# Performance work log

Hardware: AMD Instinct MI355X
Metric: run time of the kernel (lower is better)

The kernel has to match this reference:

```python
import jax, jax.numpy as jnp
import numpy as np

N = 50000
E = 800000
IN_DIM = 128
HID = 64
OUT_DIM = 1
NEG_SLOPE = 0.2
EPS = 1e-16


def _glorot(key, shape):
    fan = shape[-1] + (shape[0] if len(shape) > 1 else shape[-1])
    lim = jnp.sqrt(6.0 / fan)
    return jax.random.uniform(key, shape, jnp.float32, -lim, lim)


def setup_inputs() -> dict:
    key = jax.random.key(0)
    ks = jax.random.split(key, 12)
    x = jax.random.normal(ks[0], (N, IN_DIM), jnp.float32)
    edge_index = jax.random.randint(ks[1], (2, E), 0, N, jnp.int64)
    # GATConv layer 1: in=128, out=64, heads=4, concat=True
    W1 = _glorot(ks[2], (4 * HID, IN_DIM))
    att_src1 = _glorot(ks[3], (4, HID))
    att_dst1 = _glorot(ks[4], (4, HID))
    b1 = jnp.zeros((4 * HID,), jnp.float32)
    # GATConv layer 2: in=256, out=64, heads=1, concat=True
    W2 = _glorot(ks[5], (HID, 4 * HID))
    att_src2 = _glorot(ks[6], (1, HID))
    att_dst2 = _glorot(ks[7], (1, HID))
    b2 = jnp.zeros((HID,), jnp.float32)
    # final Linear(hidden, 1)
    fc_w = _glorot(ks[8], (OUT_DIM, HID))
    fc_b = jnp.zeros((OUT_DIM,), jnp.float32)
    return {"x": x, "edge_index": edge_index, "W1": W1, "att_src1": att_src1,
            "att_dst1": att_dst1, "b1": b1, "W2": W2, "att_src2": att_src2,
            "att_dst2": att_dst2, "b2": b2, "fc_w": fc_w, "fc_b": fc_b}


def _gat_layer(x, src, dst, W, att_src, att_dst, bias, heads, out_ch):
    n = x.shape[0]
    xt = (x @ W.T).reshape(n, heads, out_ch)          # [N, H, C]
    a_src = jnp.sum(xt * att_src[None], axis=-1)      # [N, H]
    a_dst = jnp.sum(xt * att_dst[None], axis=-1)      # [N, H]
    e = a_src[src] + a_dst[dst]                       # [E', H]
    e = jnp.where(e > 0, e, NEG_SLOPE * e)            # LeakyReLU(0.2)
    # segment softmax over incoming edges of each dst node
    m = jax.ops.segment_max(e, dst, num_segments=n)
    e = jnp.exp(e - m[dst])
    s = jax.ops.segment_sum(e, dst, num_segments=n)
    alpha = e / (s[dst] + EPS)                        # [E', H]
    msg = xt[src] * alpha[:, :, None]                 # [E', H, C]
    out = jax.ops.segment_sum(msg, dst, num_segments=n)
    return out.reshape(n, heads * out_ch) + bias


def reference(x, edge_index, W1, att_src1, att_dst1, b1,
              W2, att_src2, att_dst2, b2, fc_w, fc_b):
    n = x.shape[0]
    # PyG GATConv default: add self-loops
    loops = jnp.arange(n, dtype=edge_index.dtype)
    src = jnp.concatenate([edge_index[0], loops])
    dst = jnp.concatenate([edge_index[1], loops])
    h = jax.nn.relu(_gat_layer(x, src, dst, W1, att_src1, att_dst1, b1, 4, HID))
    h = jax.nn.relu(_gat_layer(h, src, dst, W2, att_src2, att_dst2, b2, 1, HID))
    logits = h @ fc_w.T + fc_b                        # [N, 1]
    return jax.nn.sigmoid(logits).squeeze()
```

## Files before the change

kernel.cpp:

```cpp
#include <hip/hip_runtime.h>
#include <hip/hip_bf16.h>

#define NN 50000
#define EE 800000
#define ET (NN + EE)
#define SG ((NN + 255) / 256)
#define GB1 ((NN + 63) / 64)

typedef __attribute__((ext_vector_type(8))) short short8;
typedef __attribute__((ext_vector_type(4))) short short4b;
typedef __attribute__((ext_vector_type(4))) float f32x4;

__device__ __forceinline__ float bf2f(unsigned short u) {
    union { unsigned int i; float f; } v; v.i = ((unsigned int)u) << 16; return v.f;
}
__device__ __forceinline__ unsigned short f2bf(float f) {
    __hip_bfloat16 h = __float2bfloat16(f);
    return *reinterpret_cast<unsigned short*>(&h);
}
__device__ __forceinline__ float lrelu(float e) { return fmaxf(e, 0.2f * e); }


__global__ void k_hist(const int* __restrict__ dst, int* __restrict__ cnt,
                       int* __restrict__ rank,
                       const float* __restrict__ W1, unsigned short* __restrict__ w1b,
                       const float* __restrict__ W2, unsigned short* __restrict__ w2b) {
    int t = threadIdx.x;
    int b = blockIdx.x;
    if (b < 32) {
        int j = b * 256 + t;
        float4 v = *(const float4*)(W1 + j * 4);
        short4b o;
        o[0] = (short)f2bf(v.x); o[1] = (short)f2bf(v.y);
        o[2] = (short)f2bf(v.z); o[3] = (short)f2bf(v.w);
        *(short4b*)(w1b + j * 4) = o;
    } else if (b < 48) {
        int j = (b - 32) * 256 + t;
        float4 v = *(const float4*)(W2 + j * 4);
        short4b o;
        o[0] = (short)f2bf(v.x); o[1] = (short)f2bf(v.y);
        o[2] = (short)f2bf(v.z); o[3] = (short)f2bf(v.w);
        *(short4b*)(w2b + j * 4) = o;
    }
    int i = b * blockDim.x + t;
    if (i < EE) rank[i] = atomicAdd(&cnt[dst[i]], 1);
}

__global__ __launch_bounds__(256) void k_scan1(const int* __restrict__ cnt,
                                               int* __restrict__ tmp, int* __restrict__ bsum) {
    int b = blockIdx.x, t = threadIdx.x, i = b * 256 + t;
    int lane = t & 63, w = t >> 6;
    int v = (i < NN) ? cnt[i] : 0;
    int s = v;
    #pragma unroll
    for (int off = 1; off < 64; off <<= 1) {
        int u = __shfl_up(s, off);
        if (lane >= off) s += u;
    }
    __shared__ int ws[4];
    if (lane == 63) ws[w] = s;
    __syncthreads();
    if (t == 0) {
        int a = 0;
        #pragma unroll
        for (int k = 0; k < 4; k++) { int x = ws[k]; ws[k] = a; a += x; }
        bsum[b] = a;
    }
    __syncthreads();
    s += ws[w];
    if (i < NN) tmp[i] = s;
}

__global__ __launch_bounds__(256) void k_scan2(const int* __restrict__ bsum, int* __restrict__ boff) {
    int t = threadIdx.x, lane = t & 63, w = t >> 6;
    int v = (t < SG) ? bsum[t] : 0;
    int s = v;
    #pragma unroll
    for (int off = 1; off < 64; off <<= 1) {
        int u = __shfl_up(s, off);
        if (lane >= off) s += u;
    }
    __shared__ int ws[4];
    if (lane == 63) ws[w] = s;
    __syncthreads();
    if (t == 0) {
        int a = 0;
        #pragma unroll
        for (int k = 0; k < 4; k++) { int x = ws[k]; ws[k] = a; a += x; }
    }
    __syncthreads();
    s += ws[w];
    if (t < SG) boff[t] = s - v;
}

__global__ void k_scan3_prep(const int* __restrict__ tmp, const int* __restrict__ boff,
                             int* __restrict__ rowptr, int* __restrict__ csr) {
    int i = blockIdx.x * blockDim.x + threadIdx.x;
    if (i == 0) rowptr[0] = 0;
    if (i < NN) {
        int base = boff[i >> 8];
        int incl = tmp[i] + base + i + 1;
        rowptr[i + 1] = incl;
        int excl = ((i & 255) ? tmp[i - 1] + base : base) + i;
        csr[excl] = i;
    }
}

__global__ __launch_bounds__(256) void k_scatter(
    const int* __restrict__ src, const int* __restrict__ dst,
    const int* __restrict__ rank, const int* __restrict__ rowptr,
    int* __restrict__ csr)
{
    int i4 = blockIdx.x * blockDim.x + threadIdx.x;
    if (i4 < EE / 4) {
        int base = i4 * 4;
        int4 d = *(const int4*)(dst + base);
        int4 r = *(const int4*)(rank + base);
        int4 s = *(const int4*)(src + base);
        csr[rowptr[d.x] + 1 + r.x] = s.x;
        csr[rowptr[d.y] + 1 + r.y] = s.y;
        csr[rowptr[d.z] + 1 + r.z] = s.z;
        csr[rowptr[d.w] + 1 + r.w] = s.w;
    }
}

template<int K, int N, int NH, bool A_BF16, bool B_BF16>
__device__ __forceinline__ void gemm_body(
    int bid, const void* __restrict__ Aptr, const void* __restrict__ Wptr,
    const float* __restrict__ atts, const float* __restrict__ attd,
    unsigned short* __restrict__ C, float* __restrict__ as_, float* __restrict__ ad_,
    int M)
{
    constexpr int KU  = K / 8;
    constexpr int KUH = KU / 2;
    constexpr int KC  = K / 32;
    constexpr int NW  = N / 4;
    constexpr int NI  = NW / 16;
    constexpr int ABYTES = 64 * KU * 16;
    constexpr int BBYTES = N * KUH * 16;
    constexpr int SMEM = ABYTES + BBYTES + (NH == 1 ? 2048 : 0);
    __shared__ char smem[SMEM];
    char* Ash = smem;
    char* Bsh = smem + ABYTES;
    unsigned short* Csh = (unsigned short*)smem;
    float* scsh = (float*)(smem + ABYTES + BBYTES);

    int t = threadIdx.x;
    int lane = t & 63, w = t >> 6;
    int colL = lane & 15, quad = lane >> 4;
    int m0 = bid * 64;

    {
        constexpr int CNT = 64 * KU / 256;
        #pragma unroll
        for (int i = 0; i < CNT; i++) {
            int v = t + 256 * i;
            int m = v / KU, u = v % KU;
            int gr = m0 + m; if (gr >= M) gr = M - 1;
            short8 val;
            if (A_BF16) {
                val = *(const short8*)((const unsigned short*)Aptr + (size_t)gr * K + u * 8);
            } else {
                const float* Af = (const float*)Aptr;
                float4 lo = *(const float4*)(Af + (size_t)gr * K + u * 8);
                float4 hi = *(const float4*)(Af + (size_t)gr * K + u * 8 + 4);
                val[0] = (short)f2bf(lo.x); val[1] = (short)f2bf(lo.y);
                val[2] = (short)f2bf(lo.z); val[3] = (short)f2bf(lo.w);
                val[4] = (short)f2bf(hi.x); val[5] = (short)f2bf(hi.y);
                val[6] = (short)f2bf(hi.z); val[7] = (short)f2bf(hi.w);
            }
            *(short8*)(Ash + ((size_t)m * KU + (u ^ (m & 7))) * 16) = val;
        }
    }

    f32x4 acc[4][NI];
    #pragma unroll
    for (int mi = 0; mi < 4; mi++)
        #pragma unroll
        for (int ni = 0; ni < NI; ni++) acc[mi][ni] = (f32x4){0.f, 0.f, 0.f, 0.f};

    #pragma unroll
    for (int kh = 0; kh < 2; kh++) {
        __syncthreads();
        {
            constexpr int CNT = N * KUH / 256;
            #pragma unroll
            for (int i = 0; i < CNT; i++) {
                int v = t + 256 * i;
                int n = v / KUH, uu = v % KUH;
                int u = kh * KUH + uu;
                short8 val;
                if (B_BF16) {
                    val = *(const short8*)((const unsigned short*)Wptr + (size_t)n * K + u * 8);
                } else {
                    const float* Wf = (const float*)Wptr;
                    float4 lo = *(const float4*)(Wf + (size_t)n * K + u * 8);
                    float4 hi = *(const float4*)(Wf + (size_t)n * K + u * 8 + 4);
                    val[0] = (short)f2bf(lo.x); val[1] = (short)f2bf(lo.y);
                    val[2] = (short)f2bf(lo.z); val[3] = (short)f2bf(lo.w);
                    val[4] = (short)f2bf(hi.x); val[5] = (short)f2bf(hi.y);
                    val[6] = (short)f2bf(hi.z); val[7] = (short)f2bf(hi.w);
                }
                *(short8*)(Bsh + ((size_t)n * KUH + (uu ^ (n & 7))) * 16) = val;
            }
        }
        __syncthreads();
        #pragma unroll
        for (int kcl = 0; kcl < KC / 2; kcl++) {
            int uA = (kh * (KC / 2) + kcl) * 4 + quad;
            int uB = kcl * 4 + quad;
            short8 bfr[NI];
            #pragma unroll
            for (int ni = 0; ni < NI; ni++) {
                int n = w * NW + ni * 16 + colL;
                bfr[ni] = *(const short8*)(Bsh + ((size_t)n * KUH + (uB ^ (n & 7))) * 16);
            }
            #pragma unroll
            for (int mi = 0; mi < 4; mi++) {
                int m = mi * 16 + colL;
                short8 af = *(const short8*)(Ash + ((size_t)m * KU + (uA ^ (m & 7))) * 16);
                #pragma unroll
                for (int ni = 0; ni < NI; ni++)
                    acc[mi][ni] = __builtin_amdgcn_mfma_f32_16x16x32_bf16(af, bfr[ni], acc[mi][ni], 0, 0, 0);
            }
        }
    }
    __syncthreads();

    float asv[NI], adv[NI];
    #pragma unroll
    for (int ni = 0; ni < NI; ni++) {
        int na = (NH == 4) ? (w * 64 + ni * 16 + colL) : (w * 16 + colL);
        asv[ni] = atts[na];
        adv[ni] = attd[na];
    }
    #pragma unroll
    for (int mi = 0; mi < 4; mi++) {
        float ps[4] = {0.f, 0.f, 0.f, 0.f}, pd[4] = {0.f, 0.f, 0.f, 0.f};
        #pragma unroll
        for (int ni = 0; ni < NI; ni++)
            #pragma unroll
            for (int r = 0; r < 4; r++) {
                ps[r] += acc[mi][ni][r] * asv[ni];
                pd[r] += acc[mi][ni][r] * adv[ni];
            }
        #pragma unroll
        for (int off = 1; off < 16; off <<= 1)
            #pragma unroll
            for (int r = 0; r < 4; r++) {
                ps[r] += __shfl_xor(ps[r], off);
                pd[r] += __shfl_xor(pd[r], off);
            }
        if (colL == 0) {
            #pragma unroll
            for (int r = 0; r < 4; r++) {
                int rloc = mi * 16 + quad * 4 + r;
                if (NH == 4) {
                    int row = m0 + rloc;
                    if (row < M) {
                        as_[(size_t)row * 4 + w] = ps[r];
                        ad_[(size_t)row * 4 + w] = pd[r];
                    }
                } else {
                    scsh[(w * 64 + rloc) * 2 + 0] = ps[r];
                    scsh[(w * 64 + rloc) * 2 + 1] = pd[r];
                }
            }
        }
    }

    #pragma unroll
    for (int mi = 0; mi < 4; mi++)
        #pragma unroll
        for (int ni = 0; ni < NI; ni++)
            #pragma unroll
            for (int r = 0; r < 4; r++)
                Csh[(size_t)(mi * 16 + quad * 4 + r) * (N + 8) + w * NW + ni * 16 + colL] =
                    f2bf(acc[mi][ni][r]);
    __syncthreads();

    {
        constexpr int CNT = 64 * (N / 8) / 256;
        #pragma unroll
        for (int i = 0; i < CNT; i++) {
            int v = t + 256 * i;
            int m = v / (N / 8), u = v % (N / 8);
            int row = m0 + m;
            if (row < M)
                *(short8*)(C + (size_t)row * N + u * 8) =
                    *(const short8*)(Csh + (size_t)m * (N + 8) + u * 8);
        }
    }
    if (NH == 1 && t < 64) {
        int row = m0 + t;
        if (row < M) {
            float s = 0.f, d = 0.f;
            #pragma unroll
            for (int ww = 0; ww < 4; ww++) {
                s += scsh[(ww * 64 + t) * 2 + 0];
                d += scsh[(ww * 64 + t) * 2 + 1];
            }
            as_[row] = s;
            ad_[row] = d;
        }
    }
}

template<int K, int N, int NH, bool A_BF16, bool B_BF16>
__global__ __launch_bounds__(256) void k_gemm_mfma(
    const void* __restrict__ Aptr, const void* __restrict__ Wptr,
    const float* __restrict__ atts, const float* __restrict__ attd,
    unsigned short* __restrict__ C, float* __restrict__ as_, float* __restrict__ ad_,
    int M)
{
    gemm_body<K, N, NH, A_BF16, B_BF16>(blockIdx.x, Aptr, Wptr, atts, attd, C, as_, ad_, M);
}

__global__ __launch_bounds__(256) void k_l1_agg(
    const unsigned short* __restrict__ xt1, const float* __restrict__ as1,
    const float* __restrict__ ad1, const int* __restrict__ rowptr,
    const int* __restrict__ csr, const float* __restrict__ b1,
    unsigned short* __restrict__ h1)
{
    int t = threadIdx.x;
    int lane = t & 63, w = t >> 6;
    int n = blockIdx.x * 4 + w;
    int beg = rowptr[n], deg = rowptr[n + 1] - beg;
    int half = lane >> 5, c = lane & 31, h = c >> 3;
    float adh = ad1[n * 4 + h];
    const char* xb = (const char*)xt1;
    const char* ab = (const char*)as1;
    unsigned co = (unsigned)(c << 4);
    unsigned ho = (unsigned)(h << 2);

    float acc[8] = {0.f, 0.f, 0.f, 0.f, 0.f, 0.f, 0.f, 0.f};
    float esum = 0.f;
    int j = 0;
    for (; j + 8 <= deg; j += 8) {
        int p = beg + j + half * 4;
        int s0 = csr[p], s1 = csr[p + 1], s2 = csr[p + 2], s3 = csr[p + 3];
        float a0 = *(const float*)(ab + ((unsigned)(s0 << 4) + ho));
        float a1 = *(const float*)(ab + ((unsigned)(s1 << 4) + ho));
        float a2 = *(const float*)(ab + ((unsigned)(s2 << 4) + ho));
        float a3 = *(const float*)(ab + ((unsigned)(s3 << 4) + ho));
        short8 r0 = *(const short8*)(xb + ((unsigned)(s0 << 9) + co));
        short8 r1 = *(const short8*)(xb + ((unsigned)(s1 << 9) + co));
        short8 r2 = *(const short8*)(xb + ((unsigned)(s2 << 9) + co));
        short8 r3 = *(const short8*)(xb + ((unsigned)(s3 << 9) + co));
        float e0 = __expf(lrelu(a0 + adh));
        float e1 = __expf(lrelu(a1 + adh));
        float e2 = __expf(lrelu(a2 + adh));
        float e3 = __expf(lrelu(a3 + adh));
        esum += (e0 + e1) + (e2 + e3);
        #pragma unroll
        for (int k = 0; k < 8; k++)
            acc[k] += (bf2f((unsigned short)r0[k]) * e0 + bf2f((unsigned short)r1[k]) * e1)
                    + (bf2f((unsigned short)r2[k]) * e2 + bf2f((unsigned short)r3[k]) * e3);
    }
    if (j + 4 <= deg) {
        int p = beg + j + half * 2;
        int s0 = csr[p], s1 = csr[p + 1];
        float a0 = *(const float*)(ab + ((unsigned)(s0 << 4) + ho));
        float a1 = *(const float*)(ab + ((unsigned)(s1 << 4) + ho));
        short8 r0 = *(const short8*)(xb + ((unsigned)(s0 << 9) + co));
        short8 r1 = *(const short8*)(xb + ((unsigned)(s1 << 9) + co));
        float e0 = __expf(lrelu(a0 + adh));
        float e1 = __expf(lrelu(a1 + adh));
        esum += e0 + e1;
        #pragma unroll
        for (int k = 0; k < 8; k++)
            acc[k] += bf2f((unsigned short)r0[k]) * e0 + bf2f((unsigned short)r1[k]) * e1;
        j += 4;
    }
    for (; j < deg; j += 2) {
        int jj = j + half;
        if (jj < deg) {
            int s = csr[beg + jj];
            float a0 = *(const float*)(ab + ((unsigned)(s << 4) + ho));
            short8 r = *(const short8*)(xb + ((unsigned)(s << 9) + co));
            float e = __expf(lrelu(a0 + adh));
            esum += e;
            #pragma unroll
            for (int k = 0; k < 8; k++) acc[k] += bf2f((unsigned short)r[k]) * e;
        }
    }
    #pragma unroll
    for (int k = 0; k < 8; k++) acc[k] += __shfl_xor(acc[k], 32);
    esum += __shfl_xor(esum, 32);
    if (half == 0) {
        float rs = 1.f / (esum + 1e-16f);
        float4 bl = *(const float4*)(b1 + c * 8);
        float4 bh = *(const float4*)(b1 + c * 8 + 4);
        float bb[8] = {bl.x, bl.y, bl.z, bl.w, bh.x, bh.y, bh.z, bh.w};
        short8 o;
        #pragma unroll
        for (int k = 0; k < 8; k++)
            o[k] = (short)f2bf(fmaxf(acc[k] * rs + bb[k], 0.f));
        *(short8*)(h1 + (size_t)n * 256 + c * 8) = o;
    }
}

__global__ __launch_bounds__(256) void k_l2_agg(
    const unsigned short* __restrict__ xt2, const float* __restrict__ as2,
    const float* __restrict__ ad2, const int* __restrict__ rowptr,
    const int* __restrict__ csr, const float* __restrict__ b2,
    const float* __restrict__ fcw, const float* __restrict__ fcb,
    float* __restrict__ out)
{
    int t = threadIdx.x;
    int lane = t & 63, w = t >> 6;
    int n = blockIdx.x * 4 + w;
    int beg = rowptr[n], deg = rowptr[n + 1] - beg;
    int q = lane >> 4, c = lane & 15;
    float adv = ad2[n];
    const char* xb = (const char*)xt2;
    unsigned co = (unsigned)(c << 3);

    float acc[4] = {0.f, 0.f, 0.f, 0.f};
    float esum = 0.f;
    int j = 0;
    if (deg >= 16) {
        int p = beg + q * 4;
        int s0 = csr[p], s1 = csr[p + 1], s2 = csr[p + 2], s3 = csr[p + 3];
        float a0 = as2[s0], a1 = as2[s1], a2 = as2[s2], a3 = as2[s3];
        uint2 r0 = *(const uint2*)(xb + ((unsigned)(s0 << 7) + co));
        uint2 r1 = *(const uint2*)(xb + ((unsigned)(s1 << 7) + co));
        uint2 r2 = *(const uint2*)(xb + ((unsigned)(s2 << 7) + co));
        uint2 r3 = *(const uint2*)(xb + ((unsigned)(s3 << 7) + co));
        for (; j + 32 <= deg; j += 16) {
            int p2 = beg + j + 16 + q * 4;
            int u0 = csr[p2], u1 = csr[p2 + 1], u2 = csr[p2 + 2], u3 = csr[p2 + 3];
            float f0 = as2[u0], f1 = as2[u1], f2 = as2[u2], f3 = as2[u3];
            uint2 q0 = *(const uint2*)(xb + ((unsigned)(u0 << 7) + co));
            uint2 q1 = *(const uint2*)(xb + ((unsigned)(u1 << 7) + co));
            uint2 q2 = *(const uint2*)(xb + ((unsigned)(u2 << 7) + co));
            uint2 q3 = *(const uint2*)(xb + ((unsigned)(u3 << 7) + co));
            float e0 = __expf(lrelu(a0 + adv));
            float e1 = __expf(lrelu(a1 + adv));
            float e2 = __expf(lrelu(a2 + adv));
            float e3 = __expf(lrelu(a3 + adv));
            esum += (e0 + e1) + (e2 + e3);
            acc[0] += (bf2f((unsigned short)(r0.x & 0xffff)) * e0 + bf2f((unsigned short)(r1.x & 0xffff)) * e1)
                    + (bf2f((unsigned short)(r2.x & 0xffff)) * e2 + bf2f((unsigned short)(r3.x & 0xffff)) * e3);
            acc[1] += (bf2f((unsigned short)(r0.x >> 16)) * e0 + bf2f((unsigned short)(r1.x >> 16)) * e1)
                    + (bf2f((unsigned short)(r2.x >> 16)) * e2 + bf2f((unsigned short)(r3.x >> 16)) * e3);
            acc[2] += (bf2f((unsigned short)(r0.y & 0xffff)) * e0 + bf2f((unsigned short)(r1.y & 0xffff)) * e1)
                    + (bf2f((unsigned short)(r2.y & 0xffff)) * e2 + bf2f((unsigned short)(r3.y & 0xffff)) * e3);
            acc[3] += (bf2f((unsigned short)(r0.y >> 16)) * e0 + bf2f((unsigned short)(r1.y >> 16)) * e1)
                    + (bf2f((unsigned short)(r2.y >> 16)) * e2 + bf2f((unsigned short)(r3.y >> 16)) * e3);
            a0 = f0; a1 = f1; a2 = f2; a3 = f3;
            r0 = q0; r1 = q1; r2 = q2; r3 = q3;
        }
        {
            float e0 = __expf(lrelu(a0 + adv));
            float e1 = __expf(lrelu(a1 + adv));
            float e2 = __expf(lrelu(a2 + adv));
            float e3 = __expf(lrelu(a3 + adv));
            esum += (e0 + e1) + (e2 + e3);
            acc[0] += (bf2f((unsigned short)(r0.x & 0xffff)) * e0 + bf2f((unsigned short)(r1.x & 0xffff)) * e1)
                    + (bf2f((unsigned short)(r2.x & 0xffff)) * e2 + bf2f((unsigned short)(r3.x & 0xffff)) * e3);
            acc[1] += (bf2f((unsigned short)(r0.x >> 16)) * e0 + bf2f((unsigned short)(r1.x >> 16)) * e1)
                    + (bf2f((unsigned short)(r2.x >> 16)) * e2 + bf2f((unsigned short)(r3.x >> 16)) * e3);
            acc[2] += (bf2f((unsigned short)(r0.y & 0xffff)) * e0 + bf2f((unsigned short)(r1.y & 0xffff)) * e1)
                    + (bf2f((unsigned short)(r2.y & 0xffff)) * e2 + bf2f((unsigned short)(r3.y & 0xffff)) * e3);
            acc[3] += (bf2f((unsigned short)(r0.y >> 16)) * e0 + bf2f((unsigned short)(r1.y >> 16)) * e1)
                    + (bf2f((unsigned short)(r2.y >> 16)) * e2 + bf2f((unsigned short)(r3.y >> 16)) * e3);
            j += 16;
        }
    }
    if (j + 8 <= deg) {
        int p = beg + j + q * 2;
        int s0 = csr[p], s1 = csr[p + 1];
        float a0 = as2[s0], a1 = as2[s1];
        uint2 r0 = *(const uint2*)(xb + ((unsigned)(s0 << 7) + co));
        uint2 r1 = *(const uint2*)(xb + ((unsigned)(s1 << 7) + co));
        float e0 = __expf(lrelu(a0 + adv));
        float e1 = __expf(lrelu(a1 + adv));
        esum += e0 + e1;
        acc[0] += bf2f((unsigned short)(r0.x & 0xffff)) * e0 + bf2f((unsigned short)(r1.x & 0xffff)) * e1;
        acc[1] += bf2f((unsigned short)(r0.x >> 16)) * e0 + bf2f((unsigned short)(r1.x >> 16)) * e1;
        acc[2] += bf2f((unsigned short)(r0.y & 0xffff)) * e0 + bf2f((unsigned short)(r1.y & 0xffff)) * e1;
        acc[3] += bf2f((unsigned short)(r0.y >> 16)) * e0 + bf2f((unsigned short)(r1.y >> 16)) * e1;
        j += 8;
    }
    for (; j < deg; j += 4) {
        int jj = j + q;
        if (jj < deg) {
            int s = csr[beg + jj];
            float a0 = as2[s];
            uint2 r = *(const uint2*)(xb + ((unsigned)(s << 7) + co));
            float e = __expf(lrelu(a0 + adv));
            esum += e;
            acc[0] += bf2f((unsigned short)(r.x & 0xffff)) * e;
            acc[1] += bf2f((unsigned short)(r.x >> 16)) * e;
            acc[2] += bf2f((unsigned short)(r.y & 0xffff)) * e;
            acc[3] += bf2f((unsigned short)(r.y >> 16)) * e;
        }
    }
    #pragma unroll
    for (int k = 0; k < 4; k++) {
        acc[k] += __shfl_xor(acc[k], 16);
        acc[k] += __shfl_xor(acc[k], 32);
    }
    esum += __shfl_xor(esum, 16);
    esum += __shfl_xor(esum, 32);
    float rs = 1.f / (esum + 1e-16f);
    float4 bv = *(const float4*)(b2 + c * 4);
    float4 fv = *(const float4*)(fcw + c * 4);
    float z = fmaxf(acc[0] * rs + bv.x, 0.f) * fv.x
            + fmaxf(acc[1] * rs + bv.y, 0.f) * fv.y
            + fmaxf(acc[2] * rs + bv.z, 0.f) * fv.z
            + fmaxf(acc[3] * rs + bv.w, 0.f) * fv.w;
    #pragma unroll
    for (int off = 8; off; off >>= 1) z += __shfl_xor(z, off);
    if (lane == 0) out[n] = 1.f / (1.f + __expf(-(z + fcb[0])));
}


extern "C" void kernel_launch(void* const* d_in, const int* in_sizes, int n_in,
                              void* d_out, int out_size, void* d_ws, size_t ws_size,
                              hipStream_t stream) {
    const float* x    = (const float*)d_in[0];
    const int*   ei   = (const int*)d_in[1];
    const float* W1   = (const float*)d_in[2];
    const float* as1w = (const float*)d_in[3];
    const float* ad1w = (const float*)d_in[4];
    const float* b1   = (const float*)d_in[5];
    const float* W2   = (const float*)d_in[6];
    const float* as2w = (const float*)d_in[7];
    const float* ad2w = (const float*)d_in[8];
    const float* b2   = (const float*)d_in[9];
    const float* fcw  = (const float*)d_in[10];
    const float* fcb  = (const float*)d_in[11];
    float* out = (float*)d_out;

    const int* src = ei;
    const int* dst = ei + EE;

    char* base = (char*)d_ws;
    size_t off = 0;
    auto alloc = [&](size_t bytes) -> void* {
        void* p = base + off;
        off = (off + bytes + 255) & ~(size_t)255;
        return p;
    };
    int*   rowptr   = (int*)alloc((NN + 1) * sizeof(int));
    int*   cnt      = (int*)alloc(NN * sizeof(int));
    int*   tmp      = (int*)alloc(NN * sizeof(int));
    int*   bsum     = (int*)alloc(SG * sizeof(int));
    int*   boff     = (int*)alloc(SG * sizeof(int));
    int*   rank     = (int*)alloc(EE * sizeof(int));
    int*   csr      = (int*)alloc(ET * sizeof(int));
    unsigned short* xt1 = (unsigned short*)alloc((size_t)NN * 256 * sizeof(unsigned short));
    unsigned short* h1  = (unsigned short*)alloc((size_t)NN * 256 * sizeof(unsigned short));
    unsigned short* w1b = (unsigned short*)alloc(256 * 128 * sizeof(unsigned short));
    unsigned short* w2b = (unsigned short*)alloc(64 * 256 * sizeof(unsigned short));
    float* as1      = (float*)alloc(NN * 4 * sizeof(float));
    float* ad1      = (float*)alloc(NN * 4 * sizeof(float));
    float* as2      = (float*)alloc(NN * sizeof(float));
    float* ad2      = (float*)alloc(NN * sizeof(float));
    unsigned short* xt2 = xt1;

    hipMemsetAsync(cnt, 0, NN * sizeof(int), stream);
    k_hist<<<(EE + 255) / 256, 256, 0, stream>>>(dst, cnt, rank, W1, w1b, W2, w2b);
    k_scan1<<<SG, 256, 0, stream>>>(cnt, tmp, bsum);
    k_scan2<<<1, 256, 0, stream>>>(bsum, boff);
    k_scan3_prep<<<SG, 256, 0, stream>>>(tmp, boff, rowptr, csr);
    k_scatter<<<(EE / 4 + 255) / 256, 256, 0, stream>>>(src, dst, rank, rowptr, csr);

    k_gemm_mfma<128, 256, 4, false, true><<<GB1, 256, 0, stream>>>(
        x, w1b, as1w, ad1w, xt1, as1, ad1, NN);

    k_l1_agg<<<(NN + 3) / 4, 256, 0, stream>>>(xt1, as1, ad1, rowptr, csr, b1, h1);
    k_gemm_mfma<256, 64, 1, true, true><<<GB1, 256, 0, stream>>>(
        h1, w2b, as2w, ad2w, xt2, as2, ad2, NN);
    k_l2_agg<<<(NN + 3) / 4, 256, 0, stream>>>(xt2, as2, ad2, rowptr, csr, b2, fcw, fcb, out);
}
```

Measured before the change: 268.5 us.

## Split layer-1 GEMM across histogram and scatter kernels to overlap CSR build

The layer-1 GEMM is split in half. One half runs in the same launch as the degree histogram and W2 conversion, and the other half in the same launch as the CSR scatter, with GEMM blocks and graph blocks interleaved so the memory-bound atomics overlap MFMA work. The GEMM now reads fp32 W1 directly (B_BF16=false) instead of a pre-converted bf16 copy, and the histogram processes four edges per thread. This removes two kernel launches and the W1 conversion, but the GEMM must convert B on the fly and can see resource contention with the co-scheduled atomic traffic.

```diff
diff --git a/kernel.cpp b/kernel.cpp
--- a/kernel.cpp
+++ b/kernel.cpp
@@ -6,6 +6,9 @@
 #define ET (NN + EE)
 #define SG ((NN + 255) / 256)
 #define GB1 ((NN + 63) / 64)
+#define GA  391
+#define GBB (GB1 - GA)
+#define HB  782
 
 typedef __attribute__((ext_vector_type(8))) short short8;
 typedef __attribute__((ext_vector_type(4))) short short4b;
@@ -20,31 +23,6 @@
 }
 __device__ __forceinline__ float lrelu(float e) { return fmaxf(e, 0.2f * e); }
 
-
-__global__ void k_hist(const int* __restrict__ dst, int* __restrict__ cnt,
-                       int* __restrict__ rank,
-                       const float* __restrict__ W1, unsigned short* __restrict__ w1b,
-                       const float* __restrict__ W2, unsigned short* __restrict__ w2b) {
-    int t = threadIdx.x;
-    int b = blockIdx.x;
-    if (b < 32) {
-        int j = b * 256 + t;
-        float4 v = *(const float4*)(W1 + j * 4);
-        short4b o;
-        o[0] = (short)f2bf(v.x); o[1] = (short)f2bf(v.y);
-        o[2] = (short)f2bf(v.z); o[3] = (short)f2bf(v.w);
-        *(short4b*)(w1b + j * 4) = o;
-    } else if (b < 48) {
-        int j = (b - 32) * 256 + t;
-        float4 v = *(const float4*)(W2 + j * 4);
-        short4b o;
-        o[0] = (short)f2bf(v.x); o[1] = (short)f2bf(v.y);
-        o[2] = (short)f2bf(v.z); o[3] = (short)f2bf(v.w);
-        *(short4b*)(w2b + j * 4) = o;
-    }
-    int i = b * blockDim.x + t;
-    if (i < EE) rank[i] = atomicAdd(&cnt[dst[i]], 1);
-}
 
 __global__ __launch_bounds__(256) void k_scan1(const int* __restrict__ cnt,
                                                int* __restrict__ tmp, int* __restrict__ bsum) {
@@ -103,24 +81,6 @@
         rowptr[i + 1] = incl;
         int excl = ((i & 255) ? tmp[i - 1] + base : base) + i;
         csr[excl] = i;
-    }
-}
-
-__global__ __launch_bounds__(256) void k_scatter(
-    const int* __restrict__ src, const int* __restrict__ dst,
-    const int* __restrict__ rank, const int* __restrict__ rowptr,
-    int* __restrict__ csr)
-{
-    int i4 = blockIdx.x * blockDim.x + threadIdx.x;
-    if (i4 < EE / 4) {
-        int base = i4 * 4;
-        int4 d = *(const int4*)(dst + base);
-        int4 r = *(const int4*)(rank + base);
-        int4 s = *(const int4*)(src + base);
-        csr[rowptr[d.x] + 1 + r.x] = s.x;
-        csr[rowptr[d.y] + 1 + r.y] = s.y;
-        csr[rowptr[d.z] + 1 + r.z] = s.z;
-        csr[rowptr[d.w] + 1 + r.w] = s.w;
     }
 }
 
@@ -314,6 +274,74 @@
     int M)
 {
     gemm_body<K, N, NH, A_BF16, B_BF16>(blockIdx.x, Aptr, Wptr, atts, attd, C, as_, ad_, M);
+}
+
+__global__ __launch_bounds__(256) void k_gemm1_hist(
+    const void* __restrict__ Aptr, const void* __restrict__ Wptr,
+    const float* __restrict__ atts, const float* __restrict__ attd,
+    unsigned short* __restrict__ C, float* __restrict__ as_, float* __restrict__ ad_,
+    int M,
+    const int* __restrict__ dst, int* __restrict__ cnt, int* __restrict__ rank,
+    const float* __restrict__ W2, unsigned short* __restrict__ w2b)
+{
+    int bid = blockIdx.x;
+    bool isg; int ord;
+    if (bid < 2 * GA) { isg = !(bid & 1); ord = bid >> 1; }
+    else              { isg = false;      ord = bid - GA; }
+    if (isg) {
+        gemm_body<128, 256, 4, false, false>(ord, Aptr, Wptr, atts, attd, C, as_, ad_, M);
+    } else {
+        int t = threadIdx.x;
+        if (ord < 16) {
+            int j = ord * 256 + t;
+            float4 v = *(const float4*)(W2 + j * 4);
+            short4b o;
+            o[0] = (short)f2bf(v.x); o[1] = (short)f2bf(v.y);
+            o[2] = (short)f2bf(v.z); o[3] = (short)f2bf(v.w);
+            *(short4b*)(w2b + j * 4) = o;
+        }
+        int i4 = ord * 256 + t;
+        if (i4 < EE / 4) {
+            int base = i4 * 4;
+            int4 d = *(const int4*)(dst + base);
+            int4 rr;
+            rr.x = atomicAdd(&cnt[d.x], 1);
+            rr.y = atomicAdd(&cnt[d.y], 1);
+            rr.z = atomicAdd(&cnt[d.z], 1);
+            rr.w = atomicAdd(&cnt[d.w], 1);
+            *(int4*)(rank + base) = rr;
+        }
+    }
+}
+
+__global__ __launch_bounds__(256) void k_gemm1_scatter(
+    const void* __restrict__ Aptr, const void* __restrict__ Wptr,
+    const float* __restrict__ atts, const float* __restrict__ attd,
+    unsigned short* __restrict__ C, float* __restrict__ as_, float* __restrict__ ad_,
+    int M,
+    const int* __restrict__ src, const int* __restrict__ dst,
+    const int* __restrict__ rank, const int* __restrict__ rowptr,
+    int* __restrict__ csr)
+{
+    int bid = blockIdx.x;
+    bool isg; int ord;
+    if (bid < 2 * GBB) { isg = !(bid & 1); ord = bid >> 1; }
+    else               { isg = false;      ord = bid - GBB; }
+    if (isg) {
+        gemm_body<128, 256, 4, false, false>(GA + ord, Aptr, Wptr, atts, attd, C, as_, ad_, M);
+    } else {
+        int i4 = ord * 256 + threadIdx.x;
+        if (i4 < EE / 4) {
+            int base = i4 * 4;
+            int4 d = *(const int4*)(dst + base);
+            int4 r = *(const int4*)(rank + base);
+            int4 s = *(const int4*)(src + base);
+            csr[rowptr[d.x] + 1 + r.x] = s.x;
+            csr[rowptr[d.y] + 1 + r.y] = s.y;
+            csr[rowptr[d.z] + 1 + r.z] = s.z;
+            csr[rowptr[d.w] + 1 + r.w] = s.w;
+        }
+    }
 }
 
 __global__ __launch_bounds__(256) void k_l1_agg(
@@ -553,7 +581,6 @@
     int*   csr      = (int*)alloc(ET * sizeof(int));
     unsigned short* xt1 = (unsigned short*)alloc((size_t)NN * 256 * sizeof(unsigned short));
     unsigned short* h1  = (unsigned short*)alloc((size_t)NN * 256 * sizeof(unsigned short));
-    unsigned short* w1b = (unsigned short*)alloc(256 * 128 * sizeof(unsigned short));
     unsigned short* w2b = (unsigned short*)alloc(64 * 256 * sizeof(unsigned short));
     float* as1      = (float*)alloc(NN * 4 * sizeof(float));
     float* ad1      = (float*)alloc(NN * 4 * sizeof(float));
@@ -562,14 +589,16 @@
     unsigned short* xt2 = xt1;
 
     hipMemsetAsync(cnt, 0, NN * sizeof(int), stream);
-    k_hist<<<(EE + 255) / 256, 256, 0, stream>>>(dst, cnt, rank, W1, w1b, W2, w2b);
+
+    k_gemm1_hist<<<2 * GA + (HB - GA), 256, 0, stream>>>(
+        x, W1, as1w, ad1w, xt1, as1, ad1, NN, dst, cnt, rank, W2, w2b);
+
     k_scan1<<<SG, 256, 0, stream>>>(cnt, tmp, bsum);
     k_scan2<<<1, 256, 0, stream>>>(bsum, boff);
     k_scan3_prep<<<SG, 256, 0, stream>>>(tmp, boff, rowptr, csr);
-    k_scatter<<<(EE / 4 + 255) / 256, 256, 0, stream>>>(src, dst, rank, rowptr, csr);
-
-    k_gemm_mfma<128, 256, 4, false, true><<<GB1, 256, 0, stream>>>(
-        x, w1b, as1w, ad1w, xt1, as1, ad1, NN);
+
+    k_gemm1_scatter<<<2 * GBB + (HB - GBB), 256, 0, stream>>>(
+        x, W1, as1w, ad1w, xt1, as1, ad1, NN, src, dst, rank, rowptr, csr);
 
     k_l1_agg<<<(NN + 3) / 4, 256, 0, stream>>>(xt1, as1, ad1, rowptr, csr, b1, h1);
     k_gemm_mfma<256, 64, 1, true, true><<<GB1, 256, 0, stream>>>(
```

Result: no change. 267.0 us (-0.6%).
